# Optimization experiments

Measured on AMD Instinct MI355X. Metric: run time of the kernel, lower is better.

Reference implementation:

```python
import jax, jax.numpy as jnp
import numpy as np
from jax import lax

H = 8       # heads == channel dim for conv projections
D = 64      # base_dim (per-head width)
B = 8
N = 1024
EPS = 1e-5  # BatchNorm eps (torch default)


def _bn2d(y, g, b, m, v):
    # inference-mode BatchNorm2d over channel axis 1
    inv = g / jnp.sqrt(v + EPS)
    return (y - m[None, :, None, None]) * inv[None, :, None, None] + b[None, :, None, None]


def _sepconv(xh, dw, dwb, g, bb, m, v, pw, pwb):
    # xh: [b, H, n, d] treated as NCHW; depthwise 3x3 (groups=H) + BN + pointwise 1x1
    y = lax.conv_general_dilated(xh, dw, window_strides=(1, 1),
                                 padding=((1, 1), (1, 1)),
                                 feature_group_count=H,
                                 dimension_numbers=('NCHW', 'OIHW', 'NCHW'))
    y = y + dwb[None, :, None, None]
    y = _bn2d(y, g, bb, m, v)
    # pointwise 1x1 conv == channel mix
    y = jnp.einsum('oc,bchw->bohw', pw[:, :, 0, 0], y) + pwb[None, :, None, None]
    return y


def setup_inputs() -> dict:
    key = jax.random.key(0)
    ks = jax.random.split(key, 12)
    s = 0.1
    x = jax.random.normal(ks[0], (B, N, H * D), jnp.float32)
    dw_w = jax.random.normal(ks[1], (3, H, 1, 3, 3), jnp.float32) * s
    dw_b = jax.random.normal(ks[2], (3, H), jnp.float32) * s
    bn_g = 1.0 + 0.1 * jax.random.normal(ks[3], (3, H), jnp.float32)
    bn_b = jax.random.normal(ks[4], (3, H), jnp.float32) * s
    bn_m = jnp.zeros((3, H), jnp.float32)
    bn_v = jnp.ones((3, H), jnp.float32)
    pw_w = jax.random.normal(ks[5], (3, H, H, 1, 1), jnp.float32) * s
    pw_b = jax.random.normal(ks[6], (3, H), jnp.float32) * s
    re_w = jax.random.normal(ks[7], (H, H, 1, 1), jnp.float32) * 0.3
    re_b = jax.random.normal(ks[8], (H,), jnp.float32) * s
    vn_g = 1.0 + 0.1 * jax.random.normal(ks[9], (H,), jnp.float32)
    vn_b = jax.random.normal(ks[10], (H,), jnp.float32) * s
    vn_m = jnp.zeros((H,), jnp.float32)
    vn_v = jnp.ones((H,), jnp.float32)
    out_w = jax.random.normal(ks[11], (H * D, H * D), jnp.float32) * 0.02
    out_b = jnp.zeros((H * D,), jnp.float32)
    return {"x": x, "dw_w": dw_w, "dw_b": dw_b, "bn_g": bn_g, "bn_b": bn_b,
            "bn_m": bn_m, "bn_v": bn_v, "pw_w": pw_w, "pw_b": pw_b,
            "re_w": re_w, "re_b": re_b, "vn_g": vn_g, "vn_b": vn_b,
            "vn_m": vn_m, "vn_v": vn_v, "out_w": out_w, "out_b": out_b}


def reference(x, dw_w, dw_b, bn_g, bn_b, bn_m, bn_v, pw_w, pw_b,
              re_w, re_b, vn_g, vn_b, vn_m, vn_v, out_w, out_b):
    b, n, hd = x.shape
    d = hd // H
    xh = x.reshape(b, n, H, d).transpose(0, 2, 1, 3)  # [b, h, n, d]
    q, k, v = [
        _sepconv(xh, dw_w[i], dw_b[i], bn_g[i], bn_b[i], bn_m[i], bn_v[i],
                 pw_w[i], pw_b[i])
        for i in range(3)
    ]
    scale = H ** -0.5  # note: original uses dim=heads for scale
    dots = jnp.einsum('bhid,bhjd->bhij', q, k) * scale  # [b,h,n,n]
    attn = jax.nn.softmax(dots, axis=-1)
    # re-attention: 1x1 cross-head conv + BatchNorm (reatten_scale = 1.0)
    attn = jnp.einsum('oc,bcij->boij', re_w[:, :, 0, 0], attn) + re_b[None, :, None, None]
    attn = _bn2d(attn, vn_g, vn_b, vn_m, vn_v)
    out = jnp.einsum('bhij,bhjd->bhid', attn, v)
    out = out.transpose(0, 2, 1, 3).reshape(b, n, hd)
    return out @ out_w.T + out_b
```

## Files before the change

kernel.cpp:

```cpp
#include <hip/hip_runtime.h>


#define EPS 1e-5f
#define SCALE2 0.510138584f

typedef float f32x4 __attribute__((ext_vector_type(4)));
typedef short short8 __attribute__((ext_vector_type(8)));
typedef unsigned short ushort;

#define MFMA16(a, b, c) __builtin_amdgcn_mfma_f32_16x16x32_bf16(a, b, c, 0, 0, 0)

__device__ __forceinline__ unsigned short f2bf(float f) {
  union { float f; unsigned u; } v; v.f = f;
  return (unsigned short)((v.u + 0x7FFFu + ((v.u >> 16) & 1u)) >> 16);
}
__device__ __forceinline__ float bf2f(unsigned short h) {
  union { unsigned u; float f; } v; v.u = ((unsigned)h) << 16;
  return v.f;
}
__device__ __forceinline__ int cvtpk(float lo, float hi) {
  int r;
  asm("v_cvt_pk_bf16_f32 %0, %1, %2" : "=v"(r) : "v"(lo), "v"(hi));
  return r;
}

__global__ __launch_bounds__(256) void kprep(
    const float* __restrict__ dwb, const float* __restrict__ bng,
    const float* __restrict__ bnb, const float* __restrict__ bnm,
    const float* __restrict__ bnv, const float* __restrict__ pww,
    const float* __restrict__ pwb, const float* __restrict__ rew,
    const float* __restrict__ reb, const float* __restrict__ vng,
    const float* __restrict__ vnb, const float* __restrict__ vnm,
    const float* __restrict__ vnv, const float* __restrict__ outw,
    float* __restrict__ smalls, float* __restrict__ vsum,
    float* __restrict__ lsum, ushort* __restrict__ wh,
    ushort* __restrict__ wl) {
  int g = blockIdx.x * 256 + threadIdx.x;
  if (g < 262144) {
    float v = outw[g];
    ushort hi = f2bf(v);
    wh[g] = hi;
    wl[g] = f2bf(v - bf2f(hi));
  }
  if (blockIdx.x >= 1 && blockIdx.x <= 16)
    vsum[(blockIdx.x - 1) * 256 + threadIdx.x] = 0.f;
  if (blockIdx.x >= 17 && blockIdx.x <= 272)
    lsum[(blockIdx.x - 17) * 256 + threadIdx.x] = 0.f;
  if (blockIdx.x == 0) {
    int t = threadIdx.x;
    if (t < 64) {
      int o = t >> 3, c = t & 7;
      float s = vng[o] * rsqrtf(vnv[o] + EPS);
      smalls[t] = rew[o * 8 + c] * s;
    }
    if (t < 8) {
      float s = vng[t] * rsqrtf(vnv[t] + EPS);
      smalls[64 + t] = (reb[t] - vnm[t]) * s + vnb[t];
    }
    if (t < 192) {
      int p = t >> 6, rem = t & 63, o = rem >> 3, c = rem & 7;
      float s = bng[p * 8 + c] * rsqrtf(bnv[p * 8 + c] + EPS);
      smalls[72 + t] = pww[(p * 8 + o) * 8 + c] * s;
    }
    if (t < 24) {
      int p = t / 8, o = t & 7;
      float acc = pwb[p * 8 + o];
      for (int c = 0; c < 8; ++c) {
        float s = bng[p * 8 + c] * rsqrtf(bnv[p * 8 + c] + EPS);
        acc += pww[(p * 8 + o) * 8 + c] *
               ((dwb[p * 8 + c] - bnm[p * 8 + c]) * s + bnb[p * 8 + c]);
      }
      smalls[264 + t] = acc;
    }
  }
}

__global__ __launch_bounds__(256) void kqkv(
    const float* __restrict__ x, const float* __restrict__ dww,
    const float* __restrict__ smalls,
    ushort* __restrict__ qb, ushort* __restrict__ kb,
    ushort* __restrict__ vb) {
  int t = threadIdx.x;
  int blk = blockIdx.x;
  int b = blk >> 8;
  int n0 = (blk & 255) << 2;
  int d = t & 63;
  int n = n0 + (t >> 6);
  const float* pw_eff = smalls + 72;
  const float* pwb_eff = smalls + 264;
  float y[3][8];
  for (int h = 0; h < 8; ++h) {
    float nb[3][3];
#pragma unroll
    for (int ky = 0; ky < 3; ++ky) {
      int nn = n - 1 + ky;
      bool vr = (nn >= 0) && (nn < 1024);
      const float* xp = x + ((b * 1024 + nn) * 512 + h * 64 + d);
      nb[ky][0] = (vr && d > 0) ? xp[-1] : 0.f;
      nb[ky][1] = vr ? xp[0] : 0.f;
      nb[ky][2] = (vr && d < 63) ? xp[1] : 0.f;
    }
#pragma unroll
    for (int p = 0; p < 3; ++p) {
      const float* w = dww + (p * 8 + h) * 9;
      float a = 0.f;
#pragma unroll
      for (int ky = 0; ky < 3; ++ky)
#pragma unroll
        for (int kx = 0; kx < 3; ++kx) a += w[ky * 3 + kx] * nb[ky][kx];
      y[p][h] = a;
    }
  }
#pragma unroll
  for (int p = 0; p < 3; ++p) {
#pragma unroll
    for (int o = 0; o < 8; ++o) {
      float a = pwb_eff[p * 8 + o];
#pragma unroll
      for (int c = 0; c < 8; ++c) a += pw_eff[p * 64 + o * 8 + c] * y[p][c];
      int idx = ((b * 8 + o) * 1024 + n) * 64 + d;
      if (p == 0) qb[idx] = f2bf(a * SCALE2);
      else if (p == 1) kb[idx] = f2bf(a);
      else vb[idx] = f2bf(a);
    }
  }
}

__global__ __launch_bounds__(256) void kvtrans(const ushort* __restrict__ vb,
                                               ushort* __restrict__ vt,
                                               float* __restrict__ vsum) {
  __shared__ ushort lds[64 * 65];
  __shared__ float red[256];
  int bh = blockIdx.x >> 4;
  int nt = blockIdx.x & 15;
  int t = threadIdx.x;
  const ushort* src = vb + (bh * 1024 + nt * 64) * 64;
  float part = 0.f;
#pragma unroll
  for (int it = 0; it < 16; ++it) {
    int nn = (t >> 6) + it * 4;
    int d = t & 63;
    ushort v = src[nn * 64 + d];
    part += bf2f(v);
    lds[nn * 65 + d] = v;
  }
  red[t] = part;
  __syncthreads();
  ushort* dst = vt + bh * 64 * 1024 + nt * 64;
#pragma unroll
  for (int it = 0; it < 16; ++it) {
    int d = (t >> 6) + it * 4;
    int n = t & 63;
    dst[d * 1024 + n] = lds[n * 65 + d];
  }
  if (t < 64)
    atomicAdd(&vsum[bh * 64 + t],
              red[t] + red[64 + t] + red[128 + t] + red[192 + t]);
}

__global__ __launch_bounds__(512) void kl(const ushort* __restrict__ qb,
                                          const ushort* __restrict__ kb,
                                          float* __restrict__ lsum) {
  __shared__ float lacc[1024];
  int b = blockIdx.x & 7;
  int c = (blockIdx.x >> 3) & 7;
  int jq = blockIdx.x >> 6;
  int tid = threadIdx.x;
  int w = tid >> 6, l = tid & 63;
  int lrow = l & 15, lgrp = l >> 4;
  lacc[tid] = 0.f;
  lacc[tid + 512] = 0.f;
  __syncthreads();
  const ushort* kh = kb + ((b * 8 + c) * 1024 + jq * 256 + w * 32) * 64;
  short8 Kf[2][2];
#pragma unroll
  for (int jf = 0; jf < 2; ++jf)
#pragma unroll
    for (int kc = 0; kc < 2; ++kc)
      Kf[jf][kc] = *(const short8*)(kh + (jf * 16 + lrow) * 64 + kc * 32 + lgrp * 8);
  const ushort* qh = qb + (b * 8 + c) * 65536;
  for (int ci = 0; ci < 64; ++ci) {
    f32x4 a0 = {}, a1 = {};
#pragma unroll
    for (int kc = 0; kc < 2; ++kc) {
      short8 Qf = *(const short8*)(qh + (ci * 16 + lrow) * 64 + kc * 32 + lgrp * 8);
      a0 = MFMA16(Kf[0][kc], Qf, a0);
      a1 = MFMA16(Kf[1][kc], Qf, a1);
    }
    float s = 0.f;
#pragma unroll
    for (int r = 0; r < 4; ++r) s += exp2f(a0[r]) + exp2f(a1[r]);
    s += __shfl_xor(s, 16);
    s += __shfl_xor(s, 32);
    if (lgrp == 0) atomicAdd(&lacc[ci * 16 + lrow], s);
  }
  __syncthreads();
  atomicAdd(&lsum[(b * 8 + c) * 1024 + tid], lacc[tid]);
  atomicAdd(&lsum[(b * 8 + c) * 1024 + 512 + tid], lacc[512 + tid]);
}

__global__ __launch_bounds__(512, 2) void kattn2(
    const ushort* __restrict__ qb, const ushort* __restrict__ kb,
    const ushort* __restrict__ vt, const float* __restrict__ smalls,
    const float* __restrict__ vsum, const float* __restrict__ lsum,
    ushort* __restrict__ ohi, ushort* __restrict__ olo) {
  __shared__ ushort qlds[8192];
  __shared__ ushort scr[8 * 8 * 16 * 32];
  int b = blockIdx.x & 7;
  int it = blockIdx.x >> 3;
  int i0 = it * 16;
  int tid = threadIdx.x;
  int w = tid >> 6, l = tid & 63;
  int lrow = l & 15, lgrp = l >> 4;

  {
    int e = tid * 16;
    int c = e >> 10, i = (e >> 6) & 15, d0 = e & 63;
    const ushort* src = qb + ((b * 8 + c) * 1024 + i0 + i) * 64 + d0;
    int sw = (i & 7) << 3;
    *(short8*)&qlds[c * 1024 + i * 64 + (d0 ^ sw)] = *(const short8*)src;
    *(short8*)&qlds[c * 1024 + i * 64 + ((d0 + 8) ^ sw)] = *(const short8*)(src + 8);
  }
  __syncthreads();

  float Wc[64];
#pragma unroll
  for (int z = 0; z < 64; ++z)
    Wc[z] = __builtin_bit_cast(
        float, __builtin_amdgcn_readfirstlane(
                   __builtin_bit_cast(int, smalls[z])));

  float linv[8];
#pragma unroll
  for (int c = 0; c < 8; ++c)
    linv[c] = 1.0f / lsum[(b * 8 + c) * 1024 + i0 + lrow];

  const ushort* kh = kb + b * 8 * 65536;
  const ushort* vh = vt + b * 8 * 65536;
  int qsw = (lrow & 7) << 3;
  int ssw = (lrow & 3) << 3;
  int sbase = (w * 8) * 512 + lrow * 32;

  f32x4 Oacc[8][4] = {};

  for (int ch = 0; ch < 4; ++ch) {
    int jb = w * 128 + ch * 32;
#pragma unroll
    for (int sub = 0; sub < 2; ++sub) {
      int js = jb + sub * 16;
      float m[8][4];
#pragma unroll
      for (int c = 0; c < 8; ++c) {
        f32x4 acc = {};
#pragma unroll
        for (int kc = 0; kc < 2; ++kc) {
          short8 Kf = *(const short8*)(kh + c * 65536 + (js + lrow) * 64 +
                                       kc * 32 + lgrp * 8);
          short8 Qf = *(const short8*)&qlds[c * 1024 + lrow * 64 +
                                            ((kc * 32 + lgrp * 8) ^ qsw)];
          acc = MFMA16(Kf, Qf, acc);
        }
        float p[4];
#pragma unroll
        for (int r = 0; r < 4; ++r) p[r] = exp2f(acc[r]) * linv[c];
#pragma unroll
        for (int o = 0; o < 8; ++o)
#pragma unroll
          for (int r = 0; r < 4; ++r) {
            if (c == 0) m[o][r] = Wc[o * 8] * p[r];
            else        m[o][r] += Wc[o * 8 + c] * p[r];
          }
      }
      int slot = (sub * 16 + lgrp * 4) ^ ssw;
#pragma unroll
      for (int o = 0; o < 8; ++o) {
        int w0 = cvtpk(m[o][0], m[o][1]);
        int w1 = cvtpk(m[o][2], m[o][3]);
        *(int2*)&scr[sbase + o * 512 + slot] = (int2){w0, w1};
      }
    }
    int rslot = (lgrp * 8) ^ ssw;
#pragma unroll
    for (int o = 0; o < 8; ++o) {
      short8 Af = *(const short8*)&scr[sbase + o * 512 + rslot];
#pragma unroll
      for (int nq = 0; nq < 4; ++nq) {
        short8 Vf = *(const short8*)(vh + o * 65536 + (nq * 16 + lrow) * 1024 +
                                     jb + lgrp * 8);
        Oacc[o][nq] = MFMA16(Af, Vf, Oacc[o][nq]);
      }
    }
  }

  __syncthreads();
  float* red = (float*)scr;
#pragma unroll
  for (int o = 0; o < 8; ++o) {
#pragma unroll
    for (int nq = 0; nq < 4; ++nq)
#pragma unroll
      for (int r = 0; r < 4; ++r)
        red[w * 1024 + (lgrp * 4 + r) * 64 + nq * 16 + lrow] = Oacc[o][nq][r];
    __syncthreads();
#pragma unroll
    for (int e = 0; e < 2; ++e) {
      int pos = tid + e * 512;
      int i = pos >> 6, d = pos & 63;
      float s = 0.f;
#pragma unroll
      for (int ww = 0; ww < 8; ++ww) s += red[ww * 1024 + pos];
      s += smalls[64 + o] * vsum[(b * 8 + o) * 64 + d];
      int idx = (b * 1024 + i0 + i) * 512 + o * 64 + d;
      ushort hi = f2bf(s);
      ohi[idx] = hi;
      olo[idx] = f2bf(s - bf2f(hi));
    }
    __syncthreads();
  }
}

__global__ __launch_bounds__(256) void kout(
    const ushort* __restrict__ ohi, const ushort* __restrict__ olo,
    const ushort* __restrict__ wh, const ushort* __restrict__ wl,
    const float* __restrict__ outb, float* __restrict__ out) {
  int w = threadIdx.x >> 6, l = threadIdx.x & 63;
  int lrow = l & 15, lgrp = l >> 4;
  int i0 = blockIdx.x * 128 + w * 32;
  int n0 = blockIdx.y * 64;
  f32x4 acc[2][4] = {};
  for (int kc = 0; kc < 16; ++kc) {
    short8 Ah[2], Al[2], Bh[4], Bl[4];
#pragma unroll
    for (int a = 0; a < 2; ++a) {
      int ro = (i0 + a * 16 + lrow) * 512 + kc * 32 + lgrp * 8;
      Ah[a] = *(const short8*)(ohi + ro);
      Al[a] = *(const short8*)(olo + ro);
    }
#pragma unroll
    for (int nq = 0; nq < 4; ++nq) {
      int ro = (n0 + nq * 16 + lrow) * 512 + kc * 32 + lgrp * 8;
      Bh[nq] = *(const short8*)(wh + ro);
      Bl[nq] = *(const short8*)(wl + ro);
    }
#pragma unroll
    for (int a = 0; a < 2; ++a)
#pragma unroll
      for (int nq = 0; nq < 4; ++nq) {
        acc[a][nq] = MFMA16(Ah[a], Bh[nq], acc[a][nq]);
        acc[a][nq] = MFMA16(Ah[a], Bl[nq], acc[a][nq]);
        acc[a][nq] = MFMA16(Al[a], Bh[nq], acc[a][nq]);
      }
  }
#pragma unroll
  for (int a = 0; a < 2; ++a)
#pragma unroll
    for (int nq = 0; nq < 4; ++nq)
#pragma unroll
      for (int r = 0; r < 4; ++r) {
        int row = i0 + a * 16 + lgrp * 4 + r;
        int n = n0 + nq * 16 + lrow;
        out[row * 512 + n] = acc[a][nq][r] + outb[n];
      }
}

extern "C" void kernel_launch(void* const* d_in, const int* in_sizes, int n_in,
                              void* d_out, int out_size, void* d_ws, size_t ws_size,
                              hipStream_t stream) {
  const float* x   = (const float*)d_in[0];
  const float* dww = (const float*)d_in[1];
  const float* dwb = (const float*)d_in[2];
  const float* bng = (const float*)d_in[3];
  const float* bnb = (const float*)d_in[4];
  const float* bnm = (const float*)d_in[5];
  const float* bnv = (const float*)d_in[6];
  const float* pww = (const float*)d_in[7];
  const float* pwb = (const float*)d_in[8];
  const float* rew = (const float*)d_in[9];
  const float* reb = (const float*)d_in[10];
  const float* vng = (const float*)d_in[11];
  const float* vnb = (const float*)d_in[12];
  const float* vnm = (const float*)d_in[13];
  const float* vnv = (const float*)d_in[14];
  const float* outw = (const float*)d_in[15];
  const float* outb = (const float*)d_in[16];

  char* ws = (char*)d_ws;
  const size_t MB = 1024 * 1024;
  ushort* qb  = (ushort*)(ws);
  ushort* kb  = (ushort*)(ws + 8 * MB);
  ushort* vt  = (ushort*)(ws + 16 * MB);
  ushort* vb  = (ushort*)(ws + 24 * MB);
  ushort* ohi = (ushort*)(ws + 32 * MB);
  ushort* olo = (ushort*)(ws + 40 * MB);
  ushort* wh  = (ushort*)(ws + 48 * MB);
  ushort* wl  = (ushort*)(ws + 48 * MB + 512 * 1024);
  float* smalls = (float*)(ws + 49 * MB);
  float* vsum   = (float*)(ws + 49 * MB + 4096);
  float* lsum   = (float*)(ws + 49 * MB + 8192 + 16384);

  hipLaunchKernelGGL(kprep, dim3(1024), dim3(256), 0, stream,
                     dwb, bng, bnb, bnm, bnv, pww, pwb, rew, reb, vng, vnb,
                     vnm, vnv, outw, smalls, vsum, lsum, wh, wl);
  hipLaunchKernelGGL(kqkv, dim3(2048), dim3(256), 0, stream,
                     x, dww, smalls, qb, kb, vb);
  hipLaunchKernelGGL(kvtrans, dim3(1024), dim3(256), 0, stream, vb, vt, vsum);
  hipLaunchKernelGGL(kl, dim3(256), dim3(512), 0, stream, qb, kb, lsum);
  hipLaunchKernelGGL(kattn2, dim3(512), dim3(512), 0, stream,
                     qb, kb, vt, smalls, vsum, lsum, ohi, olo);
  hipLaunchKernelGGL(kout, dim3(64, 8), dim3(256), 0, stream,
                     ohi, olo, wh, wl, outb, (float*)d_out);
}
```

Baseline: 349.3 us.

## Restructure attention kernel with 32-row tiles and LDS-staged probabilities; vectorize QKV

The attention kernel now uses 1024-thread blocks that each handle 32 query rows. The mixed probabilities for all 8 heads are staged in a 160KB dynamic LDS buffer. Each wave then computes the PV product for one output head and one half of D, which removes the cross-wave reduction. The QKV projection kernel now produces two adjacent d values per thread, accumulates the pointwise mix inside the channel loop and writes packed bf16 pairs. The lsum kernel uses per-wave LDS partials in place of LDS atomics. The new attention design needs very large LDS and allows only one block per CU, which limits latency hiding.

```diff
diff --git a/kernel.cpp b/kernel.cpp
--- a/kernel.cpp
+++ b/kernel.cpp
@@ -80,49 +80,57 @@
     const float* __restrict__ smalls,
     ushort* __restrict__ qb, ushort* __restrict__ kb,
     ushort* __restrict__ vb) {
-  int t = threadIdx.x;
-  int blk = blockIdx.x;
-  int b = blk >> 8;
-  int n0 = (blk & 255) << 2;
-  int d = t & 63;
-  int n = n0 + (t >> 6);
-  const float* pw_eff = smalls + 72;
-  const float* pwb_eff = smalls + 264;
-  float y[3][8];
-  for (int h = 0; h < 8; ++h) {
-    float nb[3][3];
+  int g = blockIdx.x * 256 + threadIdx.x;
+  int dp = g & 31;
+  int n = (g >> 5) & 1023;
+  int b = g >> 15;
+  int dd = dp * 2;
+  float m[3][8][2] = {};
+  for (int c = 0; c < 8; ++c) {
+    float win[3][4];
 #pragma unroll
     for (int ky = 0; ky < 3; ++ky) {
       int nn = n - 1 + ky;
       bool vr = (nn >= 0) && (nn < 1024);
-      const float* xp = x + ((b * 1024 + nn) * 512 + h * 64 + d);
-      nb[ky][0] = (vr && d > 0) ? xp[-1] : 0.f;
-      nb[ky][1] = vr ? xp[0] : 0.f;
-      nb[ky][2] = (vr && d < 63) ? xp[1] : 0.f;
+      int nnc = nn < 0 ? 0 : (nn > 1023 ? 1023 : nn);
+      const float* xp = x + (((b << 10) + nnc) << 9) + c * 64 + dd;
+      float e0 = (dd > 0) ? xp[-1] : 0.f;
+      float2 v = *(const float2*)xp;
+      float e3 = (dd < 62) ? xp[2] : 0.f;
+      win[ky][0] = vr ? e0 : 0.f;
+      win[ky][1] = vr ? v.x : 0.f;
+      win[ky][2] = vr ? v.y : 0.f;
+      win[ky][3] = vr ? e3 : 0.f;
     }
 #pragma unroll
     for (int p = 0; p < 3; ++p) {
-      const float* w = dww + (p * 8 + h) * 9;
-      float a = 0.f;
+      const float* wp = dww + (p * 8 + c) * 9;
+      float a0 = 0.f, a1 = 0.f;
 #pragma unroll
       for (int ky = 0; ky < 3; ++ky)
 #pragma unroll
-        for (int kx = 0; kx < 3; ++kx) a += w[ky * 3 + kx] * nb[ky][kx];
-      y[p][h] = a;
-    }
-  }
-#pragma unroll
-  for (int p = 0; p < 3; ++p) {
-#pragma unroll
-    for (int o = 0; o < 8; ++o) {
-      float a = pwb_eff[p * 8 + o];
-#pragma unroll
-      for (int c = 0; c < 8; ++c) a += pw_eff[p * 64 + o * 8 + c] * y[p][c];
-      int idx = ((b * 8 + o) * 1024 + n) * 64 + d;
-      if (p == 0) qb[idx] = f2bf(a * SCALE2);
-      else if (p == 1) kb[idx] = f2bf(a);
-      else vb[idx] = f2bf(a);
-    }
+        for (int kx = 0; kx < 3; ++kx) {
+          float wv = wp[ky * 3 + kx];
+          a0 += wv * win[ky][kx];
+          a1 += wv * win[ky][kx + 1];
+        }
+#pragma unroll
+      for (int o = 0; o < 8; ++o) {
+        float wv = smalls[72 + p * 64 + o * 8 + c];
+        m[p][o][0] += wv * a0;
+        m[p][o][1] += wv * a1;
+      }
+    }
+  }
+#pragma unroll
+  for (int o = 0; o < 8; ++o) {
+    int base = ((b * 8 + o) * 1024 + n) * 64 + dd;
+    float b0 = smalls[264 + o];
+    float b1 = smalls[272 + o];
+    float b2 = smalls[280 + o];
+    *(int*)(qb + base) = cvtpk((m[0][o][0] + b0) * SCALE2, (m[0][o][1] + b0) * SCALE2);
+    *(int*)(kb + base) = cvtpk(m[1][o][0] + b1, m[1][o][1] + b1);
+    *(int*)(vb + base) = cvtpk(m[2][o][0] + b2, m[2][o][1] + b2);
   }
 }
 
@@ -158,20 +166,20 @@
               red[t] + red[64 + t] + red[128 + t] + red[192 + t]);
 }
 
-__global__ __launch_bounds__(512) void kl(const ushort* __restrict__ qb,
+__global__ __launch_bounds__(256) void kl(const ushort* __restrict__ qb,
                                           const ushort* __restrict__ kb,
                                           float* __restrict__ lsum) {
-  __shared__ float lacc[1024];
+  __shared__ float lacc[4][1024];
   int b = blockIdx.x & 7;
   int c = (blockIdx.x >> 3) & 7;
   int jq = blockIdx.x >> 6;
   int tid = threadIdx.x;
   int w = tid >> 6, l = tid & 63;
   int lrow = l & 15, lgrp = l >> 4;
-  lacc[tid] = 0.f;
-  lacc[tid + 512] = 0.f;
+#pragma unroll
+  for (int e = 0; e < 16; ++e) ((float*)lacc)[tid + e * 256] = 0.f;
   __syncthreads();
-  const ushort* kh = kb + ((b * 8 + c) * 1024 + jq * 256 + w * 32) * 64;
+  const ushort* kh = kb + ((b * 8 + c) * 1024 + jq * 128 + w * 32) * 64;
   short8 Kf[2][2];
 #pragma unroll
   for (int jf = 0; jf < 2; ++jf)
@@ -192,36 +200,40 @@
     for (int r = 0; r < 4; ++r) s += exp2f(a0[r]) + exp2f(a1[r]);
     s += __shfl_xor(s, 16);
     s += __shfl_xor(s, 32);
-    if (lgrp == 0) atomicAdd(&lacc[ci * 16 + lrow], s);
+    if (lgrp == 0) lacc[w][ci * 16 + lrow] += s;
   }
   __syncthreads();
-  atomicAdd(&lsum[(b * 8 + c) * 1024 + tid], lacc[tid]);
-  atomicAdd(&lsum[(b * 8 + c) * 1024 + 512 + tid], lacc[512 + tid]);
-}
-
-__global__ __launch_bounds__(512, 2) void kattn2(
+#pragma unroll
+  for (int e = 0; e < 4; ++e) {
+    int i = tid + e * 256;
+    atomicAdd(&lsum[(b * 8 + c) * 1024 + i],
+              lacc[0][i] + lacc[1][i] + lacc[2][i] + lacc[3][i]);
+  }
+}
+
+__global__ __launch_bounds__(1024, 4) void kattn3(
     const ushort* __restrict__ qb, const ushort* __restrict__ kb,
     const ushort* __restrict__ vt, const float* __restrict__ smalls,
     const float* __restrict__ vsum, const float* __restrict__ lsum,
     ushort* __restrict__ ohi, ushort* __restrict__ olo) {
-  __shared__ ushort qlds[8192];
-  __shared__ ushort scr[8 * 8 * 16 * 32];
+  extern __shared__ char dyn[];
+  ushort* qlds = (ushort*)dyn;
+  ushort* plds = (ushort*)(dyn + 32768);
   int b = blockIdx.x & 7;
   int it = blockIdx.x >> 3;
-  int i0 = it * 16;
+  int i0 = it * 32;
   int tid = threadIdx.x;
   int w = tid >> 6, l = tid & 63;
   int lrow = l & 15, lgrp = l >> 4;
 
   {
     int e = tid * 16;
-    int c = e >> 10, i = (e >> 6) & 15, d0 = e & 63;
+    int c = e >> 11, i = (e >> 6) & 31, d0 = e & 63;
     const ushort* src = qb + ((b * 8 + c) * 1024 + i0 + i) * 64 + d0;
     int sw = (i & 7) << 3;
-    *(short8*)&qlds[c * 1024 + i * 64 + (d0 ^ sw)] = *(const short8*)src;
-    *(short8*)&qlds[c * 1024 + i * 64 + ((d0 + 8) ^ sw)] = *(const short8*)(src + 8);
-  }
-  __syncthreads();
+    *(short8*)&qlds[c * 2048 + i * 64 + (d0 ^ sw)] = *(const short8*)src;
+    *(short8*)&qlds[c * 2048 + i * 64 + ((d0 + 8) ^ sw)] = *(const short8*)(src + 8);
+  }
 
   float Wc[64];
 #pragma unroll
@@ -230,93 +242,96 @@
         float, __builtin_amdgcn_readfirstlane(
                    __builtin_bit_cast(int, smalls[z])));
 
-  float linv[8];
+  float linv[8][2];
 #pragma unroll
   for (int c = 0; c < 8; ++c)
-    linv[c] = 1.0f / lsum[(b * 8 + c) * 1024 + i0 + lrow];
-
-  const ushort* kh = kb + b * 8 * 65536;
-  const ushort* vh = vt + b * 8 * 65536;
-  int qsw = (lrow & 7) << 3;
-  int ssw = (lrow & 3) << 3;
-  int sbase = (w * 8) * 512 + lrow * 32;
-
-  f32x4 Oacc[8][4] = {};
-
-  for (int ch = 0; ch < 4; ++ch) {
-    int jb = w * 128 + ch * 32;
-#pragma unroll
-    for (int sub = 0; sub < 2; ++sub) {
-      int js = jb + sub * 16;
+#pragma unroll
+    for (int if2 = 0; if2 < 2; ++if2)
+      linv[c][if2] = 1.0f / lsum[(b * 8 + c) * 1024 + i0 + if2 * 16 + lrow];
+
+  int o = w >> 1, dh = w & 1;
+  f32x4 Oacc[2][2] = {};
+  __syncthreads();
+
+  for (int t = 0; t < 4; ++t) {
+    int jw = t * 256 + w * 16;
+#pragma unroll 1
+    for (int if2 = 0; if2 < 2; ++if2) {
+      int irow = if2 * 16 + lrow;
+      int qoff = (irow & 7) << 3;
       float m[8][4];
-#pragma unroll
+#pragma unroll 2
       for (int c = 0; c < 8; ++c) {
         f32x4 acc = {};
 #pragma unroll
         for (int kc = 0; kc < 2; ++kc) {
-          short8 Kf = *(const short8*)(kh + c * 65536 + (js + lrow) * 64 +
+          short8 Kf = *(const short8*)(kb + ((b * 8 + c) * 1024 + jw + lrow) * 64 +
                                        kc * 32 + lgrp * 8);
-          short8 Qf = *(const short8*)&qlds[c * 1024 + lrow * 64 +
-                                            ((kc * 32 + lgrp * 8) ^ qsw)];
+          short8 Qf = *(const short8*)&qlds[c * 2048 + irow * 64 +
+                                            ((kc * 32 + lgrp * 8) ^ qoff)];
           acc = MFMA16(Kf, Qf, acc);
         }
-        float p[4];
-#pragma unroll
-        for (int r = 0; r < 4; ++r) p[r] = exp2f(acc[r]) * linv[c];
-#pragma unroll
-        for (int o = 0; o < 8; ++o)
+        float pe[4];
+#pragma unroll
+        for (int r = 0; r < 4; ++r) pe[r] = exp2f(acc[r]) * linv[c][if2];
+#pragma unroll
+        for (int o2 = 0; o2 < 8; ++o2) {
+          float wv = Wc[o2 * 8 + c];
 #pragma unroll
           for (int r = 0; r < 4; ++r) {
-            if (c == 0) m[o][r] = Wc[o * 8] * p[r];
-            else        m[o][r] += Wc[o * 8 + c] * p[r];
+            if (c == 0) m[o2][r] = wv * pe[r];
+            else        m[o2][r] += wv * pe[r];
           }
-      }
-      int slot = (sub * 16 + lgrp * 4) ^ ssw;
-#pragma unroll
-      for (int o = 0; o < 8; ++o) {
-        int w0 = cvtpk(m[o][0], m[o][1]);
-        int w1 = cvtpk(m[o][2], m[o][3]);
-        *(int2*)&scr[sbase + o * 512 + slot] = (int2){w0, w1};
-      }
-    }
-    int rslot = (lgrp * 8) ^ ssw;
-#pragma unroll
-    for (int o = 0; o < 8; ++o) {
-      short8 Af = *(const short8*)&scr[sbase + o * 512 + rslot];
-#pragma unroll
-      for (int nq = 0; nq < 4; ++nq) {
-        short8 Vf = *(const short8*)(vh + o * 65536 + (nq * 16 + lrow) * 1024 +
-                                     jb + lgrp * 8);
-        Oacc[o][nq] = MFMA16(Af, Vf, Oacc[o][nq]);
-      }
-    }
-  }
-
-  __syncthreads();
-  float* red = (float*)scr;
-#pragma unroll
-  for (int o = 0; o < 8; ++o) {
-#pragma unroll
-    for (int nq = 0; nq < 4; ++nq)
-#pragma unroll
-      for (int r = 0; r < 4; ++r)
-        red[w * 1024 + (lgrp * 4 + r) * 64 + nq * 16 + lrow] = Oacc[o][nq][r];
+        }
+      }
+      int jslot = ((w * 16 + lgrp * 4) ^ qoff);
+#pragma unroll
+      for (int o2 = 0; o2 < 8; ++o2) {
+        int w0 = cvtpk(m[o2][0], m[o2][1]);
+        int w1 = cvtpk(m[o2][2], m[o2][3]);
+        *(int2*)&plds[o2 * 8192 + irow * 256 + jslot] = (int2){w0, w1};
+      }
+    }
     __syncthreads();
-#pragma unroll
-    for (int e = 0; e < 2; ++e) {
-      int pos = tid + e * 512;
-      int i = pos >> 6, d = pos & 63;
-      float s = 0.f;
-#pragma unroll
-      for (int ww = 0; ww < 8; ++ww) s += red[ww * 1024 + pos];
-      s += smalls[64 + o] * vsum[(b * 8 + o) * 64 + d];
-      int idx = (b * 1024 + i0 + i) * 512 + o * 64 + d;
-      ushort hi = f2bf(s);
-      ohi[idx] = hi;
-      olo[idx] = f2bf(s - bf2f(hi));
+#pragma unroll 2
+    for (int kc = 0; kc < 8; ++kc) {
+      short8 Af[2];
+#pragma unroll
+      for (int if2 = 0; if2 < 2; ++if2) {
+        int irow = if2 * 16 + lrow;
+        Af[if2] = *(const short8*)&plds[o * 8192 + irow * 256 +
+                                        ((kc * 32 + lgrp * 8) ^ ((irow & 7) << 3))];
+      }
+#pragma unroll
+      for (int df = 0; df < 2; ++df) {
+        int drow = dh * 32 + df * 16 + lrow;
+        short8 Vf = *(const short8*)(vt + ((b * 8 + o) * 64 + drow) * 1024 +
+                                     t * 256 + kc * 32 + lgrp * 8);
+#pragma unroll
+        for (int if2 = 0; if2 < 2; ++if2)
+          Oacc[if2][df] = MFMA16(Af[if2], Vf, Oacc[if2][df]);
+      }
     }
     __syncthreads();
   }
+
+  float beta = smalls[64 + o];
+#pragma unroll
+  for (int if2 = 0; if2 < 2; ++if2)
+#pragma unroll
+    for (int df = 0; df < 2; ++df) {
+      int dcol = dh * 32 + df * 16 + lrow;
+      float bv = beta * vsum[(b * 8 + o) * 64 + dcol];
+#pragma unroll
+      for (int r = 0; r < 4; ++r) {
+        int i = i0 + if2 * 16 + lgrp * 4 + r;
+        float s = Oacc[if2][df][r] + bv;
+        int idx = (b * 1024 + i) * 512 + o * 64 + dcol;
+        ushort hi = f2bf(s);
+        ohi[idx] = hi;
+        olo[idx] = f2bf(s - bf2f(hi));
+      }
+    }
 }
 
 __global__ __launch_bounds__(256) void kout(
@@ -396,16 +411,19 @@
   ushort* wl  = (ushort*)(ws + 48 * MB + 512 * 1024);
   float* smalls = (float*)(ws + 49 * MB);
   float* vsum   = (float*)(ws + 49 * MB + 4096);
-  float* lsum   = (float*)(ws + 49 * MB + 8192 + 16384);
+  float* lsum   = (float*)(ws + 49 * MB + 24576);
+
+  hipFuncSetAttribute((const void*)kattn3,
+                      hipFuncAttributeMaxDynamicSharedMemorySize, 163840);
 
   hipLaunchKernelGGL(kprep, dim3(1024), dim3(256), 0, stream,
                      dwb, bng, bnb, bnm, bnv, pww, pwb, rew, reb, vng, vnb,
                      vnm, vnv, outw, smalls, vsum, lsum, wh, wl);
-  hipLaunchKernelGGL(kqkv, dim3(2048), dim3(256), 0, stream,
+  hipLaunchKernelGGL(kqkv, dim3(1024), dim3(256), 0, stream,
                      x, dww, smalls, qb, kb, vb);
   hipLaunchKernelGGL(kvtrans, dim3(1024), dim3(256), 0, stream, vb, vt, vsum);
-  hipLaunchKernelGGL(kl, dim3(256), dim3(512), 0, stream, qb, kb, lsum);
-  hipLaunchKernelGGL(kattn2, dim3(512), dim3(512), 0, stream,
+  hipLaunchKernelGGL(kl, dim3(512), dim3(256), 0, stream, qb, kb, lsum);
+  hipLaunchKernelGGL(kattn3, dim3(256), dim3(1024), 163840, stream,
                      qb, kb, vt, smalls, vsum, lsum, ohi, olo);
   hipLaunchKernelGGL(kout, dim3(64, 8), dim3(256), 0, stream,
                      ohi, olo, wh, wl, outb, (float*)d_out);
```

After: 359.6 us. 1.03x slower.
